# Optimization experiments

Hardware: AMD Instinct MI355X
Metric: run time of the kernel (lower is better)

The kernel has to match this reference:

```python
import jax, jax.numpy as jnp
import numpy as np

N_MICRO = 500_000
MICRO_DIM = 512
MACRO_DIM = 512
N_NODES = 20_000
N_EDGES = 40_000
EPS_SOFTMAX = 1e-8
EPS_LN = 1e-5


def setup_inputs() -> dict:
    key = jax.random.key(0)
    k = jax.random.split(key, 8)
    micro_features = jax.random.normal(k[0], (N_MICRO, MICRO_DIM), dtype=jnp.float32)
    # raw in [0, N_NODES+N_EDGES+2000): first N_NODES -> node ids, next N_EDGES -> edges
    # (encoded as -id-1), rest -> -100 (ignored)
    raw = jax.random.randint(k[1], (N_MICRO,), 0, N_NODES + N_EDGES + 2000)
    micro_to_macro = jnp.where(
        raw < N_NODES, raw,
        jnp.where(raw < N_NODES + N_EDGES, -(raw - N_NODES) - 1, -100)
    ).astype(jnp.int32)
    attn_w = jax.random.normal(k[2], (MICRO_DIM,), dtype=jnp.float32) / np.sqrt(MICRO_DIM)
    attn_b = jnp.zeros((), dtype=jnp.float32)
    proj_w = jax.random.normal(k[3], (MICRO_DIM, MACRO_DIM), dtype=jnp.float32) / np.sqrt(MICRO_DIM)
    proj_b = jnp.zeros((MACRO_DIM,), dtype=jnp.float32)
    ln_g = jnp.ones((MACRO_DIM,), dtype=jnp.float32)
    ln_b = jnp.zeros((MACRO_DIM,), dtype=jnp.float32)
    return {
        "micro_features": micro_features,
        "attn_w": attn_w, "attn_b": attn_b,
        "proj_w": proj_w, "proj_b": proj_b,
        "ln_g": ln_g, "ln_b": ln_b,
        "micro_to_macro": micro_to_macro,
        "num_macro_nodes": N_NODES,
        "num_macro_edges": N_EDGES,
    }


def _segment_softmax(logits, idx, num_segments):
    m = jax.ops.segment_max(logits, idx, num_segments=num_segments)
    e = jnp.exp(logits - m[idx])
    s = jax.ops.segment_sum(e, idx, num_segments=num_segments) + EPS_SOFTMAX
    return e / s[idx]


def reference(micro_features, attn_w, attn_b, proj_w, proj_b, ln_g, ln_b,
              micro_to_macro, num_macro_nodes, num_macro_edges):
    # per-element attention logit (Linear(micro_dim, 1))
    logits = micro_features @ attn_w + attn_b  # [N]

    node_mask = micro_to_macro >= 0
    edge_mask = (micro_to_macro < 0) & (micro_to_macro != -100)

    def aggregate(mapped_idx, mask, nseg):
        # route masked-out elements to a dummy trailing segment, dropped at the end
        idx = jnp.where(mask, mapped_idx, nseg)
        w = _segment_softmax(logits, idx, nseg + 1)  # [N]
        agg = jax.ops.segment_sum(micro_features * w[:, None], idx, num_segments=nseg + 1)
        return agg[:nseg]  # [nseg, micro_dim]

    node_agg = aggregate(micro_to_macro, node_mask, num_macro_nodes)
    edge_agg = aggregate(-micro_to_macro - 1, edge_mask, num_macro_edges)

    def out_proj(x):
        h = x @ proj_w + proj_b
        mu = jnp.mean(h, axis=-1, keepdims=True)
        var = jnp.mean(jnp.square(h - mu), axis=-1, keepdims=True)
        ln = (h - mu) / jnp.sqrt(var + EPS_LN) * ln_g + ln_b
        return jax.nn.gelu(ln, approximate=False)  # torch GELU default = exact erf

    return out_proj(node_agg), out_proj(edge_agg)
```

## Files before the change

### kernel.cpp

```cpp
#include <hip/hip_runtime.h>
#include <hip/hip_bf16.h>
#include <math.h>

#define N_NODES 20000
#define N_EDGES 40000
#define N_SEG   (N_NODES + N_EDGES)
#define CAP     64
#define DIM     512

typedef __attribute__((ext_vector_type(8))) short short8;
typedef __attribute__((ext_vector_type(4))) float floatx4;

__device__ __forceinline__ unsigned short f2b(float f) {
    union { float f; unsigned int i; } v; v.f = f;
    unsigned int i = v.i;
    unsigned int r = (i + 0x7fffu + ((i >> 16) & 1u)) >> 16;
    return (unsigned short)r;
}

__global__ __launch_bounds__(256) void k_logits(
    const float* __restrict__ feat,
    const float* __restrict__ attn_w,
    const float* __restrict__ attn_b,
    const int* __restrict__ m2m,
    float* __restrict__ e_arr,
    float* __restrict__ seg_sum,
    int* __restrict__ seg_cnt,
    int* __restrict__ perm,
    int n_micro)
{
    int lane = threadIdx.x & 63;
    int row  = blockIdx.x * 4 + (threadIdx.x >> 6);
    if (row >= n_micro) return;

    const float* fr = &feat[(size_t)row * DIM + lane * 8];
    float4 w0 = *(const float4*)&attn_w[lane * 8];
    float4 w1 = *(const float4*)&attn_w[lane * 8 + 4];
    float4 f0 = *(const float4*)fr;
    float4 f1 = *(const float4*)(fr + 4);

    float p = 0.f;
    p = fmaf(f0.x, w0.x, p); p = fmaf(f0.y, w0.y, p);
    p = fmaf(f0.z, w0.z, p); p = fmaf(f0.w, w0.w, p);
    p = fmaf(f1.x, w1.x, p); p = fmaf(f1.y, w1.y, p);
    p = fmaf(f1.z, w1.z, p); p = fmaf(f1.w, w1.w, p);
#pragma unroll
    for (int d = 32; d > 0; d >>= 1) p += __shfl_xor(p, d);

    if (lane == 0) {
        float e = expf(p + attn_b[0]);
        e_arr[row] = e;
        int m = m2m[row];
        int seg = -1;
        if (m >= 0) seg = m;
        else if (m != -100) seg = N_NODES + (-m - 1);
        if (seg >= 0) {
            atomicAdd(&seg_sum[seg], e);
            int pos = atomicAdd(&seg_cnt[seg], 1);
            if (pos < CAP) perm[seg * CAP + pos] = row;
        }
    }
}

__global__ __launch_bounds__(256) void k_agg(
    const float* __restrict__ feat,
    const float* __restrict__ e_arr,
    const float* __restrict__ seg_sum,
    const int* __restrict__ seg_cnt,
    const int* __restrict__ perm,
    unsigned short* __restrict__ agg)
{
    int lane = threadIdx.x & 63;
    int seg  = blockIdx.x * 4 + (threadIdx.x >> 6);
    if (seg >= N_SEG) return;

    int cnt = seg_cnt[seg];
    if (cnt > CAP) cnt = CAP;
    float sinv = 1.0f / (seg_sum[seg] + 1e-8f);

    int   myidx = (lane < cnt) ? perm[seg * CAP + lane] : 0;
    float mye   = (lane < cnt) ? e_arr[myidx] : 0.f;

    float acc[8] = {0.f, 0.f, 0.f, 0.f, 0.f, 0.f, 0.f, 0.f};
    float4 c0 = make_float4(0, 0, 0, 0), c1 = make_float4(0, 0, 0, 0);
    if (cnt > 0) {
        int i0 = __shfl(myidx, 0);
        const float* fr = &feat[(size_t)i0 * DIM + lane * 8];
        c0 = *(const float4*)fr; c1 = *(const float4*)(fr + 4);
    }
    for (int j = 0; j < cnt; ++j) {
        float4 n0 = c0, n1 = c1;
        if (j + 1 < cnt) {
            int i1 = __shfl(myidx, j + 1);
            const float* fr = &feat[(size_t)i1 * DIM + lane * 8];
            n0 = *(const float4*)fr; n1 = *(const float4*)(fr + 4);
        }
        float w = __shfl(mye, j) * sinv;
        acc[0] = fmaf(w, c0.x, acc[0]); acc[1] = fmaf(w, c0.y, acc[1]);
        acc[2] = fmaf(w, c0.z, acc[2]); acc[3] = fmaf(w, c0.w, acc[3]);
        acc[4] = fmaf(w, c1.x, acc[4]); acc[5] = fmaf(w, c1.y, acc[5]);
        acc[6] = fmaf(w, c1.z, acc[6]); acc[7] = fmaf(w, c1.w, acc[7]);
        c0 = n0; c1 = n1;
    }
    union { unsigned short us[8]; uint4 v; } o;
#pragma unroll
    for (int k = 0; k < 8; ++k) o.us[k] = f2b(acc[k]);
    *(uint4*)&agg[(size_t)seg * DIM + lane * 8] = o.v;
}

__global__ __launch_bounds__(256) void k_transpose(
    const float* __restrict__ W,
    unsigned short* __restrict__ Wt)
{
    __shared__ float tile[64][68];
    int bx = blockIdx.x & 7, by = blockIdx.x >> 3;
    int r0 = by * 64, c0 = bx * 64;
    int t = threadIdx.x;
#pragma unroll
    for (int i = 0; i < 4; ++i) {
        int idx = i * 256 + t;
        int r = idx >> 4, ch = (idx & 15) * 4;
        *(float4*)&tile[r][ch] = *(const float4*)&W[(size_t)(r0 + r) * 512 + c0 + ch];
    }
    __syncthreads();
#pragma unroll
    for (int i = 0; i < 2; ++i) {
        int idx = i * 256 + t;
        int n = idx >> 3, kc = (idx & 7) * 8;
        union { unsigned short us[8]; uint4 v; } o;
#pragma unroll
        for (int j = 0; j < 8; ++j) o.us[j] = f2b(tile[kc + j][n]);
        *(uint4*)&Wt[(size_t)(c0 + n) * 512 + r0 + kc] = o.v;
    }
}

__global__ __launch_bounds__(256, 2) void k_proj(
    const unsigned short* __restrict__ A,
    const unsigned short* __restrict__ Wt,
    const float* __restrict__ pb,
    const float* __restrict__ lg,
    const float* __restrict__ lb,
    float* __restrict__ out)
{
    __shared__ union {
        struct { unsigned short a[32 * 40]; unsigned short b[512 * 40]; } st;
        struct { float h[16 * 516]; float ps[16][17]; float ps2[16][17];
                 float mu[16]; float rs[16]; } ep;
    } u;

    int t = threadIdx.x;
    int w = t >> 6, lane = t & 63;
    int quad = lane >> 4, l15 = lane & 15;
    int bm0 = blockIdx.x * 32;

    floatx4 acc[2][8];
#pragma unroll
    for (int mt = 0; mt < 2; ++mt)
#pragma unroll
        for (int nt = 0; nt < 8; ++nt)
            acc[mt][nt] = (floatx4){0.f, 0.f, 0.f, 0.f};

    for (int kk = 0; kk < 512; kk += 32) {
        if (t < 128) {
            int r = t >> 2, k8 = (t & 3) * 8;
            *(uint4*)&u.st.a[r * 40 + k8] = *(const uint4*)&A[(size_t)(bm0 + r) * 512 + kk + k8];
        }
#pragma unroll
        for (int i = 0; i < 8; ++i) {
            int c = i * 256 + t;
            int n = c >> 2, k8 = (c & 3) * 8;
            *(uint4*)&u.st.b[n * 40 + k8] = *(const uint4*)&Wt[(size_t)n * 512 + kk + k8];
        }
        __syncthreads();

        int kb = quad * 8;
        short8 af[2], bf[8];
#pragma unroll
        for (int mt = 0; mt < 2; ++mt)
            af[mt] = *(const short8*)&u.st.a[(mt * 16 + l15) * 40 + kb];
#pragma unroll
        for (int nt = 0; nt < 8; ++nt)
            bf[nt] = *(const short8*)&u.st.b[(w * 128 + nt * 16 + l15) * 40 + kb];
#pragma unroll
        for (int mt = 0; mt < 2; ++mt)
#pragma unroll
            for (int nt = 0; nt < 8; ++nt)
                acc[mt][nt] = __builtin_amdgcn_mfma_f32_16x16x32_bf16(af[mt], bf[nt], acc[mt][nt], 0, 0, 0);
        __syncthreads();
    }

#pragma unroll 1
    for (int mt = 0; mt < 2; ++mt) {
        __syncthreads();
#pragma unroll
        for (int nt = 0; nt < 8; ++nt) {
            int col = w * 128 + nt * 16 + l15;
            float pbv = pb[col];
#pragma unroll
            for (int r = 0; r < 4; ++r) {
                int row = quad * 4 + r;
                u.ep.h[row * 516 + col] = acc[mt][nt][r] + pbv;
            }
        }
        __syncthreads();

        {
            int row = t & 15, part = t >> 4;
            float s = 0.f, s2 = 0.f;
#pragma unroll
            for (int c4 = 0; c4 < 8; ++c4) {
                float4 v = *(const float4*)&u.ep.h[row * 516 + part * 32 + c4 * 4];
                s  += v.x + v.y + v.z + v.w;
                s2 += v.x * v.x + v.y * v.y + v.z * v.z + v.w * v.w;
            }
            u.ep.ps[part][row]  = s;
            u.ep.ps2[part][row] = s2;
        }
        __syncthreads();
        if (t < 16) {
            float S = 0.f, S2 = 0.f;
#pragma unroll
            for (int p = 0; p < 16; ++p) { S += u.ep.ps[p][t]; S2 += u.ep.ps2[p][t]; }
            float mu  = S * (1.0f / 512.0f);
            float var = S2 * (1.0f / 512.0f) - mu * mu;
            u.ep.mu[t] = mu;
            u.ep.rs[t] = rsqrtf(fmaxf(var, 0.f) + 1e-5f);
        }
        __syncthreads();

#pragma unroll
        for (int i = 0; i < 8; ++i) {
            int c = i * 256 + t;
            int r = c >> 7, c4 = (c & 127) * 4;
            float4 v = *(const float4*)&u.ep.h[r * 516 + c4];
            float mu = u.ep.mu[r], rs = u.ep.rs[r];
            float vv[4] = {v.x, v.y, v.z, v.w};
            float4 o;
            float* op = &o.x;
#pragma unroll
            for (int j = 0; j < 4; ++j) {
                float x = (vv[j] - mu) * rs * lg[c4 + j] + lb[c4 + j];
                op[j] = 0.5f * x * (1.0f + erff(x * 0.70710678118f));
            }
            *(float4*)&out[(size_t)(bm0 + mt * 16 + r) * 512 + c4] = o;
        }
    }
}

extern "C" void kernel_launch(void* const* d_in, const int* in_sizes, int n_in,
                              void* d_out, int out_size, void* d_ws, size_t ws_size,
                              hipStream_t stream)
{
    const float* feat   = (const float*)d_in[0];
    const float* attn_w = (const float*)d_in[1];
    const float* attn_b = (const float*)d_in[2];
    const float* proj_w = (const float*)d_in[3];
    const float* proj_b = (const float*)d_in[4];
    const float* ln_g   = (const float*)d_in[5];
    const float* ln_b   = (const float*)d_in[6];
    const int*   m2m    = (const int*)d_in[7];
    float* out          = (float*)d_out;

    int n_micro = in_sizes[0] / DIM;
    size_t nr = ((size_t)n_micro + 255) & ~(size_t)255;

    char* ws = (char*)d_ws;
    float* e_arr   = (float*)ws;
    float* seg_sum = e_arr + nr;
    int*   seg_cnt = (int*)(seg_sum + N_SEG);
    int*   perm    = seg_cnt + N_SEG;
    unsigned short* Wt  = (unsigned short*)(perm + (size_t)N_SEG * CAP);
    unsigned short* agg = Wt + 512 * 512;

    hipMemsetAsync(seg_sum, 0, (size_t)N_SEG * 2 * sizeof(float), stream);
    k_transpose<<<64, 256, 0, stream>>>(proj_w, Wt);
    k_logits<<<(n_micro + 3) / 4, 256, 0, stream>>>(feat, attn_w, attn_b, m2m,
                                                    e_arr, seg_sum, seg_cnt, perm, n_micro);
    k_agg<<<(N_SEG + 3) / 4, 256, 0, stream>>>(feat, e_arr, seg_sum, seg_cnt, perm, agg);
    k_proj<<<N_SEG / 32, 256, 0, stream>>>(agg, Wt, proj_b, ln_g, ln_b, out);
    (void)n_in; (void)out_size; (void)ws_size;
}
```

Measured before the change: 1.986 ms.

## Fuse transpose into logits kernel, store exp weights in perm, enlarge proj tile

Merges the weight transpose into the logits kernel as extra blocks, saving one launch. Each wavefront now computes two rows, halving the block count. The exp value is stored next to each permutation slot, so aggregation no longer gathers from a per-row array. The projection GEMM tile grows from 32 to 64 rows, raising reuse of the staged weight tile but also register use and the risk of out-of-range reads in the last partial tile.

```diff
diff --git a/kernel.cpp b/kernel.cpp
--- a/kernel.cpp
+++ b/kernel.cpp
@@ -18,56 +18,104 @@
     return (unsigned short)r;
 }
 
-__global__ __launch_bounds__(256) void k_logits(
+__global__ __launch_bounds__(256) void k_front(
     const float* __restrict__ feat,
     const float* __restrict__ attn_w,
     const float* __restrict__ attn_b,
     const int* __restrict__ m2m,
-    float* __restrict__ e_arr,
+    const float* __restrict__ W,
     float* __restrict__ seg_sum,
     int* __restrict__ seg_cnt,
     int* __restrict__ perm,
-    int n_micro)
+    float* __restrict__ eperm,
+    unsigned short* __restrict__ Wt,
+    int n_micro, int nbl)
 {
-    int lane = threadIdx.x & 63;
-    int row  = blockIdx.x * 4 + (threadIdx.x >> 6);
-    if (row >= n_micro) return;
-
-    const float* fr = &feat[(size_t)row * DIM + lane * 8];
+    __shared__ float tile[64][68];
+    int t = threadIdx.x;
+
+    if (blockIdx.x >= (unsigned)nbl) {
+        int b = blockIdx.x - nbl;
+        int bx = b & 7, by = b >> 3;
+        int r0 = by * 64, c0 = bx * 64;
+#pragma unroll
+        for (int i = 0; i < 4; ++i) {
+            int idx = i * 256 + t;
+            int r = idx >> 4, ch = (idx & 15) * 4;
+            *(float4*)&tile[r][ch] = *(const float4*)&W[(size_t)(r0 + r) * 512 + c0 + ch];
+        }
+        __syncthreads();
+#pragma unroll
+        for (int i = 0; i < 2; ++i) {
+            int idx = i * 256 + t;
+            int n = idx >> 3, kc = (idx & 7) * 8;
+            union { unsigned short us[8]; uint4 v; } o;
+#pragma unroll
+            for (int j = 0; j < 8; ++j) o.us[j] = f2b(tile[kc + j][n]);
+            *(uint4*)&Wt[(size_t)(c0 + n) * 512 + r0 + kc] = o.v;
+        }
+        return;
+    }
+
+    int lane = t & 63;
+    int row0 = (blockIdx.x * 4 + (t >> 6)) * 2;
+    if (row0 >= n_micro) return;
+    bool has1 = (row0 + 1) < n_micro;
+
     float4 w0 = *(const float4*)&attn_w[lane * 8];
     float4 w1 = *(const float4*)&attn_w[lane * 8 + 4];
-    float4 f0 = *(const float4*)fr;
-    float4 f1 = *(const float4*)(fr + 4);
-
-    float p = 0.f;
-    p = fmaf(f0.x, w0.x, p); p = fmaf(f0.y, w0.y, p);
-    p = fmaf(f0.z, w0.z, p); p = fmaf(f0.w, w0.w, p);
-    p = fmaf(f1.x, w1.x, p); p = fmaf(f1.y, w1.y, p);
-    p = fmaf(f1.z, w1.z, p); p = fmaf(f1.w, w1.w, p);
-#pragma unroll
-    for (int d = 32; d > 0; d >>= 1) p += __shfl_xor(p, d);
-
-    if (lane == 0) {
-        float e = expf(p + attn_b[0]);
-        e_arr[row] = e;
-        int m = m2m[row];
-        int seg = -1;
-        if (m >= 0) seg = m;
-        else if (m != -100) seg = N_NODES + (-m - 1);
-        if (seg >= 0) {
-            atomicAdd(&seg_sum[seg], e);
-            int pos = atomicAdd(&seg_cnt[seg], 1);
-            if (pos < CAP) perm[seg * CAP + pos] = row;
+
+    const float* fr0 = &feat[(size_t)row0 * DIM + lane * 8];
+    float4 a0 = *(const float4*)fr0;
+    float4 a1 = *(const float4*)(fr0 + 4);
+    float4 b0 = make_float4(0, 0, 0, 0), b1 = make_float4(0, 0, 0, 0);
+    if (has1) {
+        b0 = *(const float4*)(fr0 + DIM);
+        b1 = *(const float4*)(fr0 + DIM + 4);
+    }
+
+    float p0 = 0.f, p1 = 0.f;
+    p0 = fmaf(a0.x, w0.x, p0); p0 = fmaf(a0.y, w0.y, p0);
+    p0 = fmaf(a0.z, w0.z, p0); p0 = fmaf(a0.w, w0.w, p0);
+    p0 = fmaf(a1.x, w1.x, p0); p0 = fmaf(a1.y, w1.y, p0);
+    p0 = fmaf(a1.z, w1.z, p0); p0 = fmaf(a1.w, w1.w, p0);
+    p1 = fmaf(b0.x, w0.x, p1); p1 = fmaf(b0.y, w0.y, p1);
+    p1 = fmaf(b0.z, w0.z, p1); p1 = fmaf(b0.w, w0.w, p1);
+    p1 = fmaf(b1.x, w1.x, p1); p1 = fmaf(b1.y, w1.y, p1);
+    p1 = fmaf(b1.z, w1.z, p1); p1 = fmaf(b1.w, w1.w, p1);
+#pragma unroll
+    for (int d = 32; d > 0; d >>= 1) {
+        p0 += __shfl_xor(p0, d);
+        p1 += __shfl_xor(p1, d);
+    }
+
+    if ((lane & 31) == 0) {
+        int row = row0 + (lane >> 5);
+        if (row < n_micro) {
+            float pv = (lane == 0) ? p0 : p1;
+            float e = expf(pv + attn_b[0]);
+            int m = m2m[row];
+            int seg = -1;
+            if (m >= 0) seg = m;
+            else if (m != -100) seg = N_NODES + (-m - 1);
+            if (seg >= 0) {
+                atomicAdd(&seg_sum[seg], e);
+                int pos = atomicAdd(&seg_cnt[seg], 1);
+                if (pos < CAP) {
+                    perm[seg * CAP + pos]  = row;
+                    eperm[seg * CAP + pos] = e;
+                }
+            }
         }
     }
 }
 
 __global__ __launch_bounds__(256) void k_agg(
     const float* __restrict__ feat,
-    const float* __restrict__ e_arr,
     const float* __restrict__ seg_sum,
     const int* __restrict__ seg_cnt,
     const int* __restrict__ perm,
+    const float* __restrict__ eperm,
     unsigned short* __restrict__ agg)
 {
     int lane = threadIdx.x & 63;
@@ -78,8 +126,8 @@
     if (cnt > CAP) cnt = CAP;
     float sinv = 1.0f / (seg_sum[seg] + 1e-8f);
 
-    int   myidx = (lane < cnt) ? perm[seg * CAP + lane] : 0;
-    float mye   = (lane < cnt) ? e_arr[myidx] : 0.f;
+    int   myidx = (lane < cnt) ? perm[seg * CAP + lane]  : 0;
+    float mye   = (lane < cnt) ? eperm[seg * CAP + lane] : 0.f;
 
     float acc[8] = {0.f, 0.f, 0.f, 0.f, 0.f, 0.f, 0.f, 0.f};
     float4 c0 = make_float4(0, 0, 0, 0), c1 = make_float4(0, 0, 0, 0);
@@ -106,32 +154,6 @@
 #pragma unroll
     for (int k = 0; k < 8; ++k) o.us[k] = f2b(acc[k]);
     *(uint4*)&agg[(size_t)seg * DIM + lane * 8] = o.v;
-}
-
-__global__ __launch_bounds__(256) void k_transpose(
-    const float* __restrict__ W,
-    unsigned short* __restrict__ Wt)
-{
-    __shared__ float tile[64][68];
-    int bx = blockIdx.x & 7, by = blockIdx.x >> 3;
-    int r0 = by * 64, c0 = bx * 64;
-    int t = threadIdx.x;
-#pragma unroll
-    for (int i = 0; i < 4; ++i) {
-        int idx = i * 256 + t;
-        int r = idx >> 4, ch = (idx & 15) * 4;
-        *(float4*)&tile[r][ch] = *(const float4*)&W[(size_t)(r0 + r) * 512 + c0 + ch];
-    }
-    __syncthreads();
-#pragma unroll
-    for (int i = 0; i < 2; ++i) {
-        int idx = i * 256 + t;
-        int n = idx >> 3, kc = (idx & 7) * 8;
-        union { unsigned short us[8]; uint4 v; } o;
-#pragma unroll
-        for (int j = 0; j < 8; ++j) o.us[j] = f2b(tile[kc + j][n]);
-        *(uint4*)&Wt[(size_t)(c0 + n) * 512 + r0 + kc] = o.v;
-    }
 }
 
 __global__ __launch_bounds__(256, 2) void k_proj(
@@ -143,7 +165,7 @@
     float* __restrict__ out)
 {
     __shared__ union {
-        struct { unsigned short a[32 * 40]; unsigned short b[512 * 40]; } st;
+        struct { unsigned short a[64 * 40]; unsigned short b[512 * 40]; } st;
         struct { float h[16 * 516]; float ps[16][17]; float ps2[16][17];
                  float mu[16]; float rs[16]; } ep;
     } u;
@@ -151,17 +173,17 @@
     int t = threadIdx.x;
     int w = t >> 6, lane = t & 63;
     int quad = lane >> 4, l15 = lane & 15;
-    int bm0 = blockIdx.x * 32;
-
-    floatx4 acc[2][8];
-#pragma unroll
-    for (int mt = 0; mt < 2; ++mt)
+    int bm0 = blockIdx.x * 64;
+
+    floatx4 acc[4][8];
+#pragma unroll
+    for (int mt = 0; mt < 4; ++mt)
 #pragma unroll
         for (int nt = 0; nt < 8; ++nt)
             acc[mt][nt] = (floatx4){0.f, 0.f, 0.f, 0.f};
 
     for (int kk = 0; kk < 512; kk += 32) {
-        if (t < 128) {
+        {
             int r = t >> 2, k8 = (t & 3) * 8;
             *(uint4*)&u.st.a[r * 40 + k8] = *(const uint4*)&A[(size_t)(bm0 + r) * 512 + kk + k8];
         }
@@ -174,15 +196,15 @@
         __syncthreads();
 
         int kb = quad * 8;
-        short8 af[2], bf[8];
-#pragma unroll
-        for (int mt = 0; mt < 2; ++mt)
+        short8 af[4], bf[8];
+#pragma unroll
+        for (int mt = 0; mt < 4; ++mt)
             af[mt] = *(const short8*)&u.st.a[(mt * 16 + l15) * 40 + kb];
 #pragma unroll
         for (int nt = 0; nt < 8; ++nt)
             bf[nt] = *(const short8*)&u.st.b[(w * 128 + nt * 16 + l15) * 40 + kb];
 #pragma unroll
-        for (int mt = 0; mt < 2; ++mt)
+        for (int mt = 0; mt < 4; ++mt)
 #pragma unroll
             for (int nt = 0; nt < 8; ++nt)
                 acc[mt][nt] = __builtin_amdgcn_mfma_f32_16x16x32_bf16(af[mt], bf[nt], acc[mt][nt], 0, 0, 0);
@@ -190,7 +212,8 @@
     }
 
 #pragma unroll 1
-    for (int mt = 0; mt < 2; ++mt) {
+    for (int mt = 0; mt < 4; ++mt) {
+        if (bm0 + mt * 16 >= N_SEG) break;
         __syncthreads();
 #pragma unroll
         for (int nt = 0; nt < 8; ++nt) {
@@ -262,21 +285,22 @@
     float* out          = (float*)d_out;
 
     int n_micro = in_sizes[0] / DIM;
-    size_t nr = ((size_t)n_micro + 255) & ~(size_t)255;
 
     char* ws = (char*)d_ws;
-    float* e_arr   = (float*)ws;
-    float* seg_sum = e_arr + nr;
+    float* seg_sum = (float*)ws;
     int*   seg_cnt = (int*)(seg_sum + N_SEG);
     int*   perm    = seg_cnt + N_SEG;
-    unsigned short* Wt  = (unsigned short*)(perm + (size_t)N_SEG * CAP);
+    float* eperm   = (float*)(perm + (size_t)N_SEG * CAP);
+    unsigned short* Wt  = (unsigned short*)(eperm + (size_t)N_SEG * CAP);
     unsigned short* agg = Wt + 512 * 512;
 
+    int nbl = (n_micro + 7) / 8;
+
     hipMemsetAsync(seg_sum, 0, (size_t)N_SEG * 2 * sizeof(float), stream);
-    k_transpose<<<64, 256, 0, stream>>>(proj_w, Wt);
-    k_logits<<<(n_micro + 3) / 4, 256, 0, stream>>>(feat, attn_w, attn_b, m2m,
-                                                    e_arr, seg_sum, seg_cnt, perm, n_micro);
-    k_agg<<<(N_SEG + 3) / 4, 256, 0, stream>>>(feat, e_arr, seg_sum, seg_cnt, perm, agg);
-    k_proj<<<N_SEG / 32, 256, 0, stream>>>(agg, Wt, proj_b, ln_g, ln_b, out);
+    k_front<<<nbl + 64, 256, 0, stream>>>(feat, attn_w, attn_b, m2m, proj_w,
+                                          seg_sum, seg_cnt, perm, eperm, Wt,
+                                          n_micro, nbl);
+    k_agg<<<(N_SEG + 3) / 4, 256, 0, stream>>>(feat, seg_sum, seg_cnt, perm, eperm, agg);
+    k_proj<<<(N_SEG + 63) / 64, 256, 0, stream>>>(agg, Wt, proj_b, ln_g, ln_b, out);
     (void)n_in; (void)out_size; (void)ws_size;
 }
```

New measurement: 1.950 ms. About the same (-1.8%).
